# Performance work log

Measured on AMD Instinct MI355X. Metric: run time of the kernel, lower is better.

The kernel has to match this reference:

```python
import jax, jax.numpy as jnp
import numpy as np
import math

B, S, D, H = 4, 2048, 1024, 16
DK = D // H


def setup_inputs() -> dict:
    key = jax.random.key(0)
    ks = jax.random.split(key, 5)
    stdv_in = math.sqrt(3.0 / (2 * D))
    stdv_out = math.sqrt(1.0 / D)
    return {
        "query": jax.random.normal(ks[0], (B, S, D), dtype=jnp.float32),
        "key": jax.random.normal(ks[1], (B, S, D), dtype=jnp.float32),
        "value": jax.random.normal(ks[2], (B, S, D), dtype=jnp.float32),
        "input_weight": jax.random.uniform(ks[3], (3, D, D), dtype=jnp.float32, minval=-stdv_in, maxval=stdv_in),
        "output_weight": jax.random.uniform(ks[4], (D, D), dtype=jnp.float32, minval=-stdv_out, maxval=stdv_out),
    }


def reference(query, key, value, input_weight, output_weight):
    # x @ W.T, split into heads: (B,S,D) -> (B,H,S,dk)
    def proj(x, w):
        return (x @ w.T).reshape(B, S, H, DK).transpose(0, 2, 1, 3)

    q = proj(query, input_weight[0])
    k = proj(key, input_weight[1])
    v = proj(value, input_weight[2])

    scores = jnp.einsum("bhqd,bhkd->bhqk", q, k) / math.sqrt(DK)  # (B,H,S,S)
    similarity = jax.nn.softmax(scores, axis=-1)
    attn = jnp.einsum("bhqk,bhkd->bhqd", similarity, v)  # (B,H,S,dk)
    attn = attn.transpose(0, 2, 1, 3).reshape(B, S, D)
    attn = attn @ output_weight.T
    # mean_simi_across_heads=True default
    sim_mean = jnp.mean(similarity, axis=1)  # (B,S,S)
    return attn, sim_mean
```

## Files before the change

### kernel.cpp

```cpp
#include <hip/hip_runtime.h>

typedef _Float16 f16x8 __attribute__((ext_vector_type(8)));
typedef _Float16 f16x4 __attribute__((ext_vector_type(4)));
typedef _Float16 f16x2 __attribute__((ext_vector_type(2)));
typedef __fp16 h16x2 __attribute__((ext_vector_type(2)));
typedef float f32x4 __attribute__((ext_vector_type(4)));

#define SWB(row, c8) ((((row) << 3) + (((c8) ^ ((row) & 7)))) << 3)

__device__ __forceinline__ float exp2_fast(float x) {
  return __builtin_amdgcn_exp2f(x);
}

__device__ __forceinline__ f16x2 pkrtz(float a, float b) {
  h16x2 r = __builtin_amdgcn_cvt_pkrtz(a, b);
  return *(f16x2*)&r;
}

__device__ __forceinline__ f16x8 pack8(float4 f0, float4 f1) {
  f16x2 p0 = pkrtz(f0.x, f0.y);
  f16x2 p1 = pkrtz(f0.z, f0.w);
  f16x2 p2 = pkrtz(f1.x, f1.y);
  f16x2 p3 = pkrtz(f1.z, f1.w);
  f16x4 a = __builtin_shufflevector(p0, p1, 0, 1, 2, 3);
  f16x4 b = __builtin_shufflevector(p2, p3, 0, 1, 2, 3);
  return __builtin_shufflevector(a, b, 0, 1, 2, 3, 4, 5, 6, 7);
}

#define LOG2E 1.44269504088896340736f

__global__ __launch_bounds__(256) void conv_kernel(
    const float* __restrict__ q, const float* __restrict__ k,
    const float* __restrict__ v, const float* __restrict__ w_in,
    const float* __restrict__ w_out, _Float16* __restrict__ Xc,
    _Float16* __restrict__ W16, float qscale) {
  int t = blockIdx.x * 256 + threadIdx.x;
  if (t < 3145728) {
    int plane = t >> 20, off = t & 1048575;
    const float* src = (plane == 0 ? q : (plane == 1 ? k : v)) + (size_t)off * 8;
    float4 f0 = *(const float4*)src;
    float4 f1 = *(const float4*)(src + 4);
    *(f16x8*)&Xc[(size_t)t * 8] = pack8(f0, f1);
  } else {
    int t2 = t - 3145728;
    int plane = t2 >> 17, off = t2 & 131071;
    const float* src = (plane < 3 ? w_in + (size_t)plane * 1048576 : w_out) + (size_t)off * 8;
    float sc = (plane == 0) ? qscale : 1.0f;
    float4 f0 = *(const float4*)src;
    float4 f1 = *(const float4*)(src + 4);
    f0.x *= sc; f0.y *= sc; f0.z *= sc; f0.w *= sc;
    f1.x *= sc; f1.y *= sc; f1.z *= sc; f1.w *= sc;
    *(f16x8*)&W16[(size_t)t2 * 8] = pack8(f0, f1);
  }
}

template <int EPI>
__global__ __launch_bounds__(256) void gemm_kernel(const _Float16* __restrict__ A0,
                                                   const _Float16* __restrict__ W16,
                                                   void* Oq, void* Ok, void* Ov) {
  __shared__ _Float16 As[128 * 64];
  __shared__ _Float16 Bs[128 * 64];
  const int tid = threadIdx.x;
  const int w = tid >> 6, lane = tid & 63, quad = lane >> 4, l16 = lane & 15;
  const int m0 = blockIdx.y * 128, n0 = blockIdx.x * 128;
  const int z = blockIdx.z;
  const int wm = (w & 1) * 64, wn = (w >> 1) * 64;
  const int srow = tid >> 3, c8 = tid & 7;

  const _Float16* A = (EPI == 0) ? A0 + (size_t)z * 8388608 : A0;
  const _Float16* W = (EPI == 0) ? W16 + (size_t)z * 1048576 : W16 + (size_t)3 * 1048576;

  f32x4 acc[4][4];
#pragma unroll
  for (int i = 0; i < 4; i++)
#pragma unroll
    for (int j = 0; j < 4; j++) acc[i][j] = (f32x4){0.f, 0.f, 0.f, 0.f};

  f16x8 pa[4], pb[4];
#pragma unroll
  for (int u = 0; u < 4; u++) {
    pa[u] = *(const f16x8*)&A[(size_t)(m0 + srow + 32 * u) * 1024 + c8 * 8];
    pb[u] = *(const f16x8*)&W[(size_t)(n0 + srow + 32 * u) * 1024 + c8 * 8];
  }
#pragma unroll
  for (int u = 0; u < 4; u++) {
    *(f16x8*)&As[SWB(srow + 32 * u, c8)] = pa[u];
    *(f16x8*)&Bs[SWB(srow + 32 * u, c8)] = pb[u];
  }

  for (int k0 = 0; k0 < 1024; k0 += 64) {
    __syncthreads();
    if (k0 < 960) {
      int kn = k0 + 64;
#pragma unroll
      for (int u = 0; u < 4; u++) {
        pa[u] = *(const f16x8*)&A[(size_t)(m0 + srow + 32 * u) * 1024 + kn + c8 * 8];
        pb[u] = *(const f16x8*)&W[(size_t)(n0 + srow + 32 * u) * 1024 + kn + c8 * 8];
      }
    }
    f16x8 af[2][4], bf[2][4];
#pragma unroll
    for (int kf = 0; kf < 2; kf++)
#pragma unroll
      for (int i = 0; i < 4; i++) {
        af[kf][i] = *(f16x8*)&As[SWB(wm + i * 16 + l16, kf * 4 + quad)];
        bf[kf][i] = *(f16x8*)&Bs[SWB(wn + i * 16 + l16, kf * 4 + quad)];
      }
#pragma unroll
    for (int kf = 0; kf < 2; kf++)
#pragma unroll
      for (int i = 0; i < 4; i++)
#pragma unroll
        for (int j = 0; j < 4; j++)
          acc[i][j] = __builtin_amdgcn_mfma_f32_16x16x32_f16(af[kf][i], bf[kf][j], acc[i][j], 0, 0, 0);
    __syncthreads();
    if (k0 < 960) {
#pragma unroll
      for (int u = 0; u < 4; u++) {
        *(f16x8*)&As[SWB(srow + 32 * u, c8)] = pa[u];
        *(f16x8*)&Bs[SWB(srow + 32 * u, c8)] = pb[u];
      }
    }
  }

  if (EPI == 1) {
    float* o = (float*)Oq;
#pragma unroll
    for (int i = 0; i < 4; i++)
#pragma unroll
      for (int j = 0; j < 4; j++)
#pragma unroll
        for (int r = 0; r < 4; r++) {
          int mg = m0 + wm + i * 16 + quad * 4 + r;
          int ng = n0 + wn + j * 16 + l16;
          o[(size_t)mg * 1024 + ng] = acc[i][j][r];
        }
  } else {
    _Float16* o = (_Float16*)(z == 0 ? Oq : (z == 1 ? Ok : Ov));
#pragma unroll
    for (int i = 0; i < 4; i++)
#pragma unroll
      for (int j = 0; j < 4; j++) {
        if (z < 2) {
#pragma unroll
          for (int r = 0; r < 4; r++) {
            int mg = m0 + wm + i * 16 + quad * 4 + r;
            int ng = n0 + wn + j * 16 + l16;
            int bb = mg >> 11, ss = mg & 2047, hh = ng >> 6, dd = ng & 63;
            o[((size_t)(bb * 16 + hh) << 17) + ss * 64 + dd] = (_Float16)acc[i][j][r];
          }
        } else {
          int mg0 = m0 + wm + i * 16 + quad * 4;
          int ng = n0 + wn + j * 16 + l16;
          int bb = mg0 >> 11, ss0 = mg0 & 2047, hh = ng >> 6, dd = ng & 63;
          f16x4 pk;
#pragma unroll
          for (int r = 0; r < 4; r++) pk[r] = (_Float16)acc[i][j][r];
          *(f16x4*)&o[((size_t)(bb * 16 + hh) << 17) + (size_t)dd * 2048 + ss0] = pk;
        }
      }
  }
}

__global__ __launch_bounds__(256) void attn_kernel(const _Float16* __restrict__ Q,
                                                   const _Float16* __restrict__ K,
                                                   const _Float16* __restrict__ Vt,
                                                   _Float16* __restrict__ O,
                                                   float* __restrict__ rl) {
  __shared__ _Float16 KtS[2 * 64 * 64];
  __shared__ _Float16 VtS[2 * 64 * 64];
  const int tid = threadIdx.x;
  const int w = tid >> 6, lane = tid & 63, quad = lane >> 4, l16 = lane & 15;
  const int h = blockIdx.y, b = blockIdx.z;
  const size_t base = (size_t)(b * 16 + h) << 17;
  const _Float16* Qh = Q + base;
  const _Float16* Kh = K + base;
  const _Float16* Vth = Vt + base;
  const int q0 = blockIdx.x * 128;
  const int wq = q0 + w * 32;
  const int c0 = tid, c1 = tid + 256;
  const int r0 = c0 >> 3, c80 = c0 & 7, r1 = c1 >> 3, c81 = c1 & 7;
  const int vA0 = (c80 >> 2) * 4 + (c80 & 1) * 2, vh0 = ((c80 >> 1) & 1) * 4;
  const int vA1 = (c81 >> 2) * 4 + (c81 & 1) * 2, vh1 = ((c81 >> 1) & 1) * 4;

  f16x8 aq[2][2];
#pragma unroll
  for (int i = 0; i < 2; i++)
#pragma unroll
    for (int kf = 0; kf < 2; kf++)
      aq[i][kf] = *(const f16x8*)&Qh[(size_t)(wq + i * 16 + l16) * 64 + kf * 32 + quad * 8];

  f32x4 accO[2][4];
  f32x4 accL[2];
#pragma unroll
  for (int i = 0; i < 2; i++) {
    accL[i] = (f32x4){0.f, 0.f, 0.f, 0.f};
#pragma unroll
    for (int j = 0; j < 4; j++) accO[i][j] = (f32x4){0.f, 0.f, 0.f, 0.f};
  }
  const f32x4 zero4 = (f32x4){0.f, 0.f, 0.f, 0.f};
  const f16x8 ones8 = (f16x8){(_Float16)1.f, (_Float16)1.f, (_Float16)1.f, (_Float16)1.f,
                              (_Float16)1.f, (_Float16)1.f, (_Float16)1.f, (_Float16)1.f};

  f16x8 kreg[2], vreg[2];
  auto loadkv = [&](int t) {
    int n0 = t * 64;
    kreg[0] = *(const f16x8*)&Kh[(size_t)(n0 + r0) * 64 + c80 * 8];
    kreg[1] = *(const f16x8*)&Kh[(size_t)(n0 + r1) * 64 + c81 * 8];
    vreg[0] = *(const f16x8*)&Vth[(size_t)r0 * 2048 + n0 + c80 * 8];
    vreg[1] = *(const f16x8*)&Vth[(size_t)r1 * 2048 + n0 + c81 * 8];
  };
  auto stage = [&](_Float16* Kb, _Float16* Vb) {
    *(f16x8*)&Kb[SWB(r0, c80)] = kreg[0];
    *(f16x8*)&Kb[SWB(r1, c81)] = kreg[1];
    f16x4 lo0 = __builtin_shufflevector(vreg[0], vreg[0], 0, 1, 2, 3);
    f16x4 hi0 = __builtin_shufflevector(vreg[0], vreg[0], 4, 5, 6, 7);
    *(f16x4*)&Vb[SWB(r0, vA0) + vh0] = lo0;
    *(f16x4*)&Vb[SWB(r0, vA0 + 1) + vh0] = hi0;
    f16x4 lo1 = __builtin_shufflevector(vreg[1], vreg[1], 0, 1, 2, 3);
    f16x4 hi1 = __builtin_shufflevector(vreg[1], vreg[1], 4, 5, 6, 7);
    *(f16x4*)&Vb[SWB(r1, vA1) + vh1] = lo1;
    *(f16x4*)&Vb[SWB(r1, vA1 + 1) + vh1] = hi1;
  };
  auto compute = [&](const _Float16* Kb, const _Float16* Vb) {
    f16x8 bk[4][2];
#pragma unroll
    for (int jj = 0; jj < 4; jj++)
#pragma unroll
      for (int kf = 0; kf < 2; kf++)
        bk[jj][kf] = *(const f16x8*)&Kb[SWB(jj * 16 + l16, kf * 4 + quad)];
    f32x4 sv[2][4];
#pragma unroll
    for (int i = 0; i < 2; i++)
#pragma unroll
      for (int jj = 0; jj < 4; jj++) {
        f32x4 t = __builtin_amdgcn_mfma_f32_16x16x32_f16(bk[jj][0], aq[i][0], zero4, 0, 0, 0);
        sv[i][jj] = __builtin_amdgcn_mfma_f32_16x16x32_f16(bk[jj][1], aq[i][1], t, 0, 0, 0);
      }
    f16x8 ap[2][2];
#pragma unroll
    for (int i = 0; i < 2; i++) {
#pragma unroll
      for (int kf = 0; kf < 2; kf++) {
        float4 e0, e1;
        e0.x = exp2_fast(sv[i][2 * kf][0]);
        e0.y = exp2_fast(sv[i][2 * kf][1]);
        e0.z = exp2_fast(sv[i][2 * kf][2]);
        e0.w = exp2_fast(sv[i][2 * kf][3]);
        e1.x = exp2_fast(sv[i][2 * kf + 1][0]);
        e1.y = exp2_fast(sv[i][2 * kf + 1][1]);
        e1.z = exp2_fast(sv[i][2 * kf + 1][2]);
        e1.w = exp2_fast(sv[i][2 * kf + 1][3]);
        ap[i][kf] = pack8(e0, e1);
      }
      accL[i] = __builtin_amdgcn_mfma_f32_16x16x32_f16(ap[i][0], ones8, accL[i], 0, 0, 0);
      accL[i] = __builtin_amdgcn_mfma_f32_16x16x32_f16(ap[i][1], ones8, accL[i], 0, 0, 0);
    }
    f16x8 bv[4][2];
#pragma unroll
    for (int jd = 0; jd < 4; jd++)
#pragma unroll
      for (int kf = 0; kf < 2; kf++)
        bv[jd][kf] = *(const f16x8*)&Vb[SWB(jd * 16 + l16, kf * 4 + quad)];
#pragma unroll
    for (int i = 0; i < 2; i++)
#pragma unroll
      for (int jd = 0; jd < 4; jd++) {
        accO[i][jd] = __builtin_amdgcn_mfma_f32_16x16x32_f16(ap[i][0], bv[jd][0], accO[i][jd], 0, 0, 0);
        accO[i][jd] = __builtin_amdgcn_mfma_f32_16x16x32_f16(ap[i][1], bv[jd][1], accO[i][jd], 0, 0, 0);
      }
  };

  loadkv(0);
  stage(&KtS[0], &VtS[0]);
  loadkv(1);
  for (int it2 = 0; it2 < 16; ++it2) {
    __syncthreads();
    stage(&KtS[4096], &VtS[4096]);
    if (it2 < 15) loadkv(2 * it2 + 2);
    compute(&KtS[0], &VtS[0]);
    __syncthreads();
    if (it2 < 15) {
      stage(&KtS[0], &VtS[0]);
      loadkv(2 * it2 + 3);
    }
    compute(&KtS[4096], &VtS[4096]);
  }

  float rinv[2][4];
#pragma unroll
  for (int i = 0; i < 2; i++)
#pragma unroll
    for (int r = 0; r < 4; r++) rinv[i][r] = 1.0f / accL[i][r];
  if (l16 == 0) {
#pragma unroll
    for (int i = 0; i < 2; i++)
#pragma unroll
      for (int r = 0; r < 4; r++)
        rl[(b * 16 + h) * 2048 + wq + i * 16 + quad * 4 + r] = rinv[i][r];
  }
#pragma unroll
  for (int i = 0; i < 2; i++)
#pragma unroll
    for (int jd = 0; jd < 4; jd++)
#pragma unroll
      for (int r = 0; r < 4; r++) {
        int rowq = wq + i * 16 + quad * 4 + r;
        O[(size_t)(b * 2048 + rowq) * 1024 + h * 64 + jd * 16 + l16] =
            (_Float16)(accO[i][jd][r] * rinv[i][r]);
      }
}

__global__ __launch_bounds__(512) void sim_kernel(const _Float16* __restrict__ Q,
                                                  const _Float16* __restrict__ K,
                                                  const float* __restrict__ rl,
                                                  float* __restrict__ out) {
  __shared__ _Float16 Ks[2 * 128 * 64];
  const int tid = threadIdx.x;
  const int w = tid >> 6, lane = tid & 63, quad = lane >> 4, l16 = lane & 15;
  const int n0 = blockIdx.x * 128, q0 = blockIdx.y * 128, b = blockIdx.z;
  const f32x4 zero4 = (f32x4){0.f, 0.f, 0.f, 0.f};
  const int c0 = tid, c1 = tid + 512;
  const int r0 = c0 >> 3, c80 = c0 & 7, r1 = c1 >> 3, c81 = c1 & 7;

  f32x4 acc[8];
#pragma unroll
  for (int jj = 0; jj < 8; jj++) acc[jj] = (f32x4){0.f, 0.f, 0.f, 0.f};

  f16x8 kreg[2];
  auto loadK = [&](int hh) {
    const size_t kb = (size_t)(b * 16 + hh) << 17;
    kreg[0] = *(const f16x8*)&K[kb + (size_t)(n0 + r0) * 64 + c80 * 8];
    kreg[1] = *(const f16x8*)&K[kb + (size_t)(n0 + r1) * 64 + c81 * 8];
  };
  auto stageK = [&](_Float16* Kb) {
    *(f16x8*)&Kb[SWB(r0, c80)] = kreg[0];
    *(f16x8*)&Kb[SWB(r1, c81)] = kreg[1];
  };
  auto computeS = [&](int hh, const _Float16* Kb) {
    const size_t qb = ((size_t)(b * 16 + hh) << 17) + (size_t)(q0 + w * 16 + l16) * 64;
    f16x8 aq0 = *(const f16x8*)&Q[qb + quad * 8];
    f16x8 aq1 = *(const f16x8*)&Q[qb + 32 + quad * 8];
    float rv[4];
#pragma unroll
    for (int r = 0; r < 4; r++)
      rv[r] = rl[(b * 16 + hh) * 2048 + q0 + w * 16 + quad * 4 + r];
#pragma unroll
    for (int jj = 0; jj < 8; jj++) {
      f16x8 b0 = *(const f16x8*)&Kb[SWB(jj * 16 + l16, quad)];
      f16x8 b1 = *(const f16x8*)&Kb[SWB(jj * 16 + l16, 4 + quad)];
      f32x4 sv = __builtin_amdgcn_mfma_f32_16x16x32_f16(aq0, b0, zero4, 0, 0, 0);
      sv = __builtin_amdgcn_mfma_f32_16x16x32_f16(aq1, b1, sv, 0, 0, 0);
#pragma unroll
      for (int r = 0; r < 4; r++) acc[jj][r] += exp2_fast(sv[r]) * rv[r];
    }
  };

  loadK(0);
  stageK(&Ks[0]);
  loadK(1);
  for (int h2 = 0; h2 < 8; ++h2) {
    __syncthreads();
    stageK(&Ks[8192]);
    if (h2 < 7) loadK(2 * h2 + 2);
    computeS(2 * h2, &Ks[0]);
    __syncthreads();
    if (h2 < 7) {
      stageK(&Ks[0]);
      loadK(2 * h2 + 3);
    }
    computeS(2 * h2 + 1, &Ks[8192]);
  }
#pragma unroll
  for (int jj = 0; jj < 8; jj++)
#pragma unroll
    for (int r = 0; r < 4; r++) {
      int rowq = q0 + w * 16 + quad * 4 + r;
      out[(size_t)(b * 2048 + rowq) * 2048 + n0 + jj * 16 + l16] = acc[jj][r] * 0.0625f;
    }
}

extern "C" void kernel_launch(void* const* d_in, const int* in_sizes, int n_in,
                              void* d_out, int out_size, void* d_ws, size_t ws_size,
                              hipStream_t stream) {
  const float* q = (const float*)d_in[0];
  const float* k = (const float*)d_in[1];
  const float* v = (const float*)d_in[2];
  const float* w_in = (const float*)d_in[3];
  const float* w_out = (const float*)d_in[4];

  _Float16* Qw = (_Float16*)d_ws;
  _Float16* Kw = Qw + 8388608;
  _Float16* Vt = Kw + 8388608;
  _Float16* Ow = Vt + 8388608;
  float* rlw = (float*)(Ow + 8388608);

  float* out_attn = (float*)d_out;
  float* out_sim = out_attn + 8388608;
  _Float16* Xc = (_Float16*)out_sim;
  _Float16* W16 = Xc + 3 * 8388608;

  conv_kernel<<<14336, 256, 0, stream>>>(q, k, v, w_in, w_out, Xc, W16,
                                         0.125f * LOG2E);
  gemm_kernel<0><<<dim3(8, 64, 3), 256, 0, stream>>>(Xc, W16, Qw, Kw, Vt);
  attn_kernel<<<dim3(16, 16, 4), 256, 0, stream>>>(Qw, Kw, Vt, Ow, rlw);
  gemm_kernel<1><<<dim3(8, 64, 1), 256, 0, stream>>>(Ow, W16, out_attn, nullptr, nullptr);
  sim_kernel<<<dim3(16, 16, 4), 512, 0, stream>>>(Qw, Kw, rlw, out_sim);
}
```

Measured before the change: 435.2 us.

## Drop LDS staging in attention and sim kernels; load K/V fragments directly from global

Both the attention and similarity kernels stop staging K/V tiles through double-buffered shared memory with barriers. Each wave now loads its MFMA operand fragments straight from global memory and relies on L1/L2 caching. The V-transpose store in the projection kernel is permuted so that the per-lane 8-element V loads come out in the fragment order the MFMA expects. Launch bounds are raised to four blocks per CU to add occupancy for hiding latency, at the cost of redundant global/L2 traffic across waves and no explicit prefetch.

```diff
diff --git a/kernel.cpp b/kernel.cpp
--- a/kernel.cpp
+++ b/kernel.cpp
@@ -153,22 +153,21 @@
           int mg0 = m0 + wm + i * 16 + quad * 4;
           int ng = n0 + wn + j * 16 + l16;
           int bb = mg0 >> 11, ss0 = mg0 & 2047, hh = ng >> 6, dd = ng & 63;
+          int sp = (ss0 & ~63) | ((i >> 1) << 5) | (quad << 3) | ((i & 1) << 2);
           f16x4 pk;
 #pragma unroll
           for (int r = 0; r < 4; r++) pk[r] = (_Float16)acc[i][j][r];
-          *(f16x4*)&o[((size_t)(bb * 16 + hh) << 17) + (size_t)dd * 2048 + ss0] = pk;
+          *(f16x4*)&o[((size_t)(bb * 16 + hh) << 17) + (size_t)dd * 2048 + sp] = pk;
         }
       }
   }
 }
 
-__global__ __launch_bounds__(256) void attn_kernel(const _Float16* __restrict__ Q,
-                                                   const _Float16* __restrict__ K,
-                                                   const _Float16* __restrict__ Vt,
-                                                   _Float16* __restrict__ O,
-                                                   float* __restrict__ rl) {
-  __shared__ _Float16 KtS[2 * 64 * 64];
-  __shared__ _Float16 VtS[2 * 64 * 64];
+__global__ __launch_bounds__(256, 4) void attn_kernel(const _Float16* __restrict__ Q,
+                                                      const _Float16* __restrict__ K,
+                                                      const _Float16* __restrict__ Vt,
+                                                      _Float16* __restrict__ O,
+                                                      float* __restrict__ rl) {
   const int tid = threadIdx.x;
   const int w = tid >> 6, lane = tid & 63, quad = lane >> 4, l16 = lane & 15;
   const int h = blockIdx.y, b = blockIdx.z;
@@ -178,10 +177,6 @@
   const _Float16* Vth = Vt + base;
   const int q0 = blockIdx.x * 128;
   const int wq = q0 + w * 32;
-  const int c0 = tid, c1 = tid + 256;
-  const int r0 = c0 >> 3, c80 = c0 & 7, r1 = c1 >> 3, c81 = c1 & 7;
-  const int vA0 = (c80 >> 2) * 4 + (c80 & 1) * 2, vh0 = ((c80 >> 1) & 1) * 4;
-  const int vA1 = (c81 >> 2) * 4 + (c81 & 1) * 2, vh1 = ((c81 >> 1) & 1) * 4;
 
   f16x8 aq[2][2];
 #pragma unroll
@@ -202,33 +197,14 @@
   const f16x8 ones8 = (f16x8){(_Float16)1.f, (_Float16)1.f, (_Float16)1.f, (_Float16)1.f,
                               (_Float16)1.f, (_Float16)1.f, (_Float16)1.f, (_Float16)1.f};
 
-  f16x8 kreg[2], vreg[2];
-  auto loadkv = [&](int t) {
-    int n0 = t * 64;
-    kreg[0] = *(const f16x8*)&Kh[(size_t)(n0 + r0) * 64 + c80 * 8];
-    kreg[1] = *(const f16x8*)&Kh[(size_t)(n0 + r1) * 64 + c81 * 8];
-    vreg[0] = *(const f16x8*)&Vth[(size_t)r0 * 2048 + n0 + c80 * 8];
-    vreg[1] = *(const f16x8*)&Vth[(size_t)r1 * 2048 + n0 + c81 * 8];
-  };
-  auto stage = [&](_Float16* Kb, _Float16* Vb) {
-    *(f16x8*)&Kb[SWB(r0, c80)] = kreg[0];
-    *(f16x8*)&Kb[SWB(r1, c81)] = kreg[1];
-    f16x4 lo0 = __builtin_shufflevector(vreg[0], vreg[0], 0, 1, 2, 3);
-    f16x4 hi0 = __builtin_shufflevector(vreg[0], vreg[0], 4, 5, 6, 7);
-    *(f16x4*)&Vb[SWB(r0, vA0) + vh0] = lo0;
-    *(f16x4*)&Vb[SWB(r0, vA0 + 1) + vh0] = hi0;
-    f16x4 lo1 = __builtin_shufflevector(vreg[1], vreg[1], 0, 1, 2, 3);
-    f16x4 hi1 = __builtin_shufflevector(vreg[1], vreg[1], 4, 5, 6, 7);
-    *(f16x4*)&Vb[SWB(r1, vA1) + vh1] = lo1;
-    *(f16x4*)&Vb[SWB(r1, vA1 + 1) + vh1] = hi1;
-  };
-  auto compute = [&](const _Float16* Kb, const _Float16* Vb) {
+  for (int it = 0; it < 32; ++it) {
+    const int nb = it * 64;
     f16x8 bk[4][2];
 #pragma unroll
     for (int jj = 0; jj < 4; jj++)
 #pragma unroll
       for (int kf = 0; kf < 2; kf++)
-        bk[jj][kf] = *(const f16x8*)&Kb[SWB(jj * 16 + l16, kf * 4 + quad)];
+        bk[jj][kf] = *(const f16x8*)&Kh[(size_t)(nb + jj * 16 + l16) * 64 + kf * 32 + quad * 8];
     f32x4 sv[2][4];
 #pragma unroll
     for (int i = 0; i < 2; i++)
@@ -237,6 +213,12 @@
         f32x4 t = __builtin_amdgcn_mfma_f32_16x16x32_f16(bk[jj][0], aq[i][0], zero4, 0, 0, 0);
         sv[i][jj] = __builtin_amdgcn_mfma_f32_16x16x32_f16(bk[jj][1], aq[i][1], t, 0, 0, 0);
       }
+    f16x8 bv[4][2];
+#pragma unroll
+    for (int jd = 0; jd < 4; jd++)
+#pragma unroll
+      for (int kf = 0; kf < 2; kf++)
+        bv[jd][kf] = *(const f16x8*)&Vth[(size_t)(jd * 16 + l16) * 2048 + nb + kf * 32 + quad * 8];
     f16x8 ap[2][2];
 #pragma unroll
     for (int i = 0; i < 2; i++) {
@@ -256,12 +238,6 @@
       accL[i] = __builtin_amdgcn_mfma_f32_16x16x32_f16(ap[i][0], ones8, accL[i], 0, 0, 0);
       accL[i] = __builtin_amdgcn_mfma_f32_16x16x32_f16(ap[i][1], ones8, accL[i], 0, 0, 0);
     }
-    f16x8 bv[4][2];
-#pragma unroll
-    for (int jd = 0; jd < 4; jd++)
-#pragma unroll
-      for (int kf = 0; kf < 2; kf++)
-        bv[jd][kf] = *(const f16x8*)&Vb[SWB(jd * 16 + l16, kf * 4 + quad)];
 #pragma unroll
     for (int i = 0; i < 2; i++)
 #pragma unroll
@@ -269,22 +245,6 @@
         accO[i][jd] = __builtin_amdgcn_mfma_f32_16x16x32_f16(ap[i][0], bv[jd][0], accO[i][jd], 0, 0, 0);
         accO[i][jd] = __builtin_amdgcn_mfma_f32_16x16x32_f16(ap[i][1], bv[jd][1], accO[i][jd], 0, 0, 0);
       }
-  };
-
-  loadkv(0);
-  stage(&KtS[0], &VtS[0]);
-  loadkv(1);
-  for (int it2 = 0; it2 < 16; ++it2) {
-    __syncthreads();
-    stage(&KtS[4096], &VtS[4096]);
-    if (it2 < 15) loadkv(2 * it2 + 2);
-    compute(&KtS[0], &VtS[0]);
-    __syncthreads();
-    if (it2 < 15) {
-      stage(&KtS[0], &VtS[0]);
-      loadkv(2 * it2 + 3);
-    }
-    compute(&KtS[4096], &VtS[4096]);
   }
 
   float rinv[2][4];
@@ -311,65 +271,38 @@
       }
 }
 
-__global__ __launch_bounds__(512) void sim_kernel(const _Float16* __restrict__ Q,
-                                                  const _Float16* __restrict__ K,
-                                                  const float* __restrict__ rl,
-                                                  float* __restrict__ out) {
-  __shared__ _Float16 Ks[2 * 128 * 64];
+__global__ __launch_bounds__(512, 4) void sim_kernel(const _Float16* __restrict__ Q,
+                                                     const _Float16* __restrict__ K,
+                                                     const float* __restrict__ rl,
+                                                     float* __restrict__ out) {
   const int tid = threadIdx.x;
   const int w = tid >> 6, lane = tid & 63, quad = lane >> 4, l16 = lane & 15;
   const int n0 = blockIdx.x * 128, q0 = blockIdx.y * 128, b = blockIdx.z;
   const f32x4 zero4 = (f32x4){0.f, 0.f, 0.f, 0.f};
-  const int c0 = tid, c1 = tid + 512;
-  const int r0 = c0 >> 3, c80 = c0 & 7, r1 = c1 >> 3, c81 = c1 & 7;
 
   f32x4 acc[8];
 #pragma unroll
   for (int jj = 0; jj < 8; jj++) acc[jj] = (f32x4){0.f, 0.f, 0.f, 0.f};
 
-  f16x8 kreg[2];
-  auto loadK = [&](int hh) {
-    const size_t kb = (size_t)(b * 16 + hh) << 17;
-    kreg[0] = *(const f16x8*)&K[kb + (size_t)(n0 + r0) * 64 + c80 * 8];
-    kreg[1] = *(const f16x8*)&K[kb + (size_t)(n0 + r1) * 64 + c81 * 8];
-  };
-  auto stageK = [&](_Float16* Kb) {
-    *(f16x8*)&Kb[SWB(r0, c80)] = kreg[0];
-    *(f16x8*)&Kb[SWB(r1, c81)] = kreg[1];
-  };
-  auto computeS = [&](int hh, const _Float16* Kb) {
-    const size_t qb = ((size_t)(b * 16 + hh) << 17) + (size_t)(q0 + w * 16 + l16) * 64;
+  for (int h = 0; h < 16; ++h) {
+    const size_t kb = (size_t)(b * 16 + h) << 17;
+    const size_t qb = kb + (size_t)(q0 + w * 16 + l16) * 64;
     f16x8 aq0 = *(const f16x8*)&Q[qb + quad * 8];
     f16x8 aq1 = *(const f16x8*)&Q[qb + 32 + quad * 8];
     float rv[4];
 #pragma unroll
     for (int r = 0; r < 4; r++)
-      rv[r] = rl[(b * 16 + hh) * 2048 + q0 + w * 16 + quad * 4 + r];
+      rv[r] = rl[(b * 16 + h) * 2048 + q0 + w * 16 + quad * 4 + r];
 #pragma unroll
     for (int jj = 0; jj < 8; jj++) {
-      f16x8 b0 = *(const f16x8*)&Kb[SWB(jj * 16 + l16, quad)];
-      f16x8 b1 = *(const f16x8*)&Kb[SWB(jj * 16 + l16, 4 + quad)];
+      const size_t krow = kb + (size_t)(n0 + jj * 16 + l16) * 64;
+      f16x8 b0 = *(const f16x8*)&K[krow + quad * 8];
+      f16x8 b1 = *(const f16x8*)&K[krow + 32 + quad * 8];
       f32x4 sv = __builtin_amdgcn_mfma_f32_16x16x32_f16(aq0, b0, zero4, 0, 0, 0);
       sv = __builtin_amdgcn_mfma_f32_16x16x32_f16(aq1, b1, sv, 0, 0, 0);
 #pragma unroll
       for (int r = 0; r < 4; r++) acc[jj][r] += exp2_fast(sv[r]) * rv[r];
     }
-  };
-
-  loadK(0);
-  stageK(&Ks[0]);
-  loadK(1);
-  for (int h2 = 0; h2 < 8; ++h2) {
-    __syncthreads();
-    stageK(&Ks[8192]);
-    if (h2 < 7) loadK(2 * h2 + 2);
-    computeS(2 * h2, &Ks[0]);
-    __syncthreads();
-    if (h2 < 7) {
-      stageK(&Ks[0]);
-      loadK(2 * h2 + 3);
-    }
-    computeS(2 * h2 + 1, &Ks[8192]);
   }
 #pragma unroll
   for (int jj = 0; jj < 8; jj++)
```

Measured after the change: 776.5 us. 78.4% more time.
